# Kernel tuning notes

Measured on AMD Instinct MI355X. Metric: run time of the kernel, lower is better.

The kernel has to match this reference:

```python
import jax, jax.numpy as jnp
import numpy as np

B, V, J, NB = 512, 6890, 24, 10
P = (J - 1) * 9  # 207 pose-blendshape features

# Standard SMPL kinematic tree (root parent = -1)
SMPL_PARENTS = np.array([-1, 0, 0, 0, 1, 2, 3, 4, 5, 6, 7, 8, 9, 9, 9,
                         12, 13, 14, 16, 17, 18, 19, 20, 21], dtype=np.int32)


def setup_inputs() -> dict:
    key = jax.random.key(0)
    ks = jax.random.split(key, 7)
    betas = jax.random.normal(ks[0], (B, NB), jnp.float32)
    pose = 0.2 * jax.random.normal(ks[1], (B, J * 3), jnp.float32)
    v_template = jax.random.normal(ks[2], (V, 3), jnp.float32)
    shapedirs = 0.01 * jax.random.normal(ks[3], (V, 3, NB), jnp.float32)
    posedirs = 0.01 * jax.random.normal(ks[4], (P, V * 3), jnp.float32)
    J_regressor = jax.random.uniform(ks[5], (J, V), jnp.float32)
    J_regressor = J_regressor / jnp.sum(J_regressor, axis=1, keepdims=True)
    lbs_weights = jax.random.uniform(ks[6], (V, J), jnp.float32)
    lbs_weights = lbs_weights / jnp.sum(lbs_weights, axis=1, keepdims=True)
    parents = jnp.asarray(SMPL_PARENTS)
    return {"betas": betas, "pose": pose, "v_template": v_template,
            "shapedirs": shapedirs, "posedirs": posedirs,
            "J_regressor": J_regressor, "lbs_weights": lbs_weights,
            "parents": parents}


def batch_rodrigues(aa):
    """Axis-angle (N,3) -> rotation matrices (N,3,3), matching the torch impl."""
    angle = jnp.linalg.norm(aa + 1e-8, axis=1, keepdims=True)  # (N,1)
    rd = aa / angle
    cos = jnp.cos(angle)[:, :, None]  # (N,1,1)
    sin = jnp.sin(angle)[:, :, None]
    rx, ry, rz = rd[:, 0], rd[:, 1], rd[:, 2]
    zeros = jnp.zeros_like(rx)
    K = jnp.stack([zeros, -rz, ry,
                   rz, zeros, -rx,
                   -ry, rx, zeros], axis=1).reshape(-1, 3, 3)
    ident = jnp.eye(3, dtype=aa.dtype)
    return ident + sin * K + (1.0 - cos) * jnp.matmul(K, K)


def reference(betas, pose, v_template, shapedirs, posedirs, J_regressor,
              lbs_weights, parents):
    par = np.asarray(parents)  # static kinematic tree (host constants)
    b = betas.shape[0]
    nj = J_regressor.shape[0]
    # shape blendshapes: v_shaped = v_template + sum_l betas_l * shapedirs[...,l]
    v_shaped = v_template[None] + jnp.einsum('bl,vkl->bvk', betas, shapedirs)
    Jloc = jnp.einsum('bvk,jv->bjk', v_shaped, J_regressor)  # (b,J,3)
    rot = batch_rodrigues(pose.reshape(-1, 3)).reshape(b, nj, 3, 3)
    # pose blendshapes
    ident = jnp.eye(3, dtype=rot.dtype)
    pose_feature = (rot[:, 1:] - ident).reshape(b, -1)  # (b,207)
    v_posed = v_shaped + (pose_feature @ posedirs).reshape(b, -1, 3)
    # relative joint locations
    rel = Jloc.at[:, 1:].add(-Jloc[:, par[1:]])
    # per-joint local transforms (b,J,4,4)
    top = jnp.concatenate([rot, rel[..., None]], axis=-1)  # (b,J,3,4)
    bottom = jnp.broadcast_to(jnp.array([0., 0., 0., 1.], dtype=rot.dtype),
                              (b, nj, 1, 4))
    tm = jnp.concatenate([top, bottom], axis=2)
    # kinematic chain (fixed, tiny loop over 24 joints with static parents)
    chain = [tm[:, 0]]
    for i in range(1, par.shape[0]):
        chain.append(chain[par[i]] @ tm[:, i])
    transforms = jnp.stack(chain, axis=1)  # (b,J,4,4) absolute transforms
    posed_joints = transforms[:, :, :3, 3]
    # remove rest-pose joint offset: A = transforms - [0|transforms @ [J;0]]
    jh = jnp.concatenate([Jloc, jnp.zeros_like(Jloc[..., :1])], axis=-1)
    init_bone = jnp.einsum('bjpq,bjq->bjp', transforms, jh)  # (b,J,4)
    A = transforms - jnp.pad(init_bone[..., None], ((0, 0), (0, 0), (0, 0), (3, 0)))
    # linear blend skinning: per-vertex transform T = sum_j w_vj * A_j
    T = jnp.einsum('vj,bjpq->bvpq', lbs_weights, A)  # (b,V,4,4)
    verts = jnp.einsum('bvpk,bvk->bvp', T[:, :, :3, :3], v_posed) + T[:, :, :3, 3]
    return verts, posed_joints, A, transforms, v_posed
```

## Files before the change

### kernel.cpp

```cpp
#include <hip/hip_runtime.h>
#include <hip/hip_bf16.h>

#define BB 512
#define VV 6890
#define NJ 24
#define NBETA 10
#define NP 207
#define N3 (VV*3)
#define TBAT 32

#define OFF_VERTS 0
#define OFF_PJ   (BB*VV*3)
#define OFF_A    (OFF_PJ + BB*NJ*3)
#define OFF_TF   (OFF_A + BB*NJ*16)
#define OFF_VP   (OFF_TF + BB*NJ*16)

#define WS_JTJS 0
#define WS_PF   (WS_JTJS + NJ*33)
#define WS_A    (WS_PF + BB*NP)

__constant__ int c_par[NJ] = {-1, 0, 0, 0, 1, 2, 3, 4, 5, 6, 7, 8,
                              9, 9, 9, 12, 13, 14, 16, 17, 18, 19, 20, 21};

__global__ void k_jreg(const float* __restrict__ jr,
                       const float* __restrict__ vt,
                       const float* __restrict__ sd,
                       float* __restrict__ ws) {
    int j = blockIdx.x / 33, idx = blockIdx.x % 33;
    int t = threadIdx.x;
    float acc = 0.f;
    for (int v = t; v < VV; v += 256) {
        float a = jr[j * VV + v];
        float x = (idx < 3) ? vt[v * 3 + idx] : sd[v * 30 + (idx - 3)];
        acc += a * x;
    }
    __shared__ float red[256];
    red[t] = acc;
    __syncthreads();
    for (int s = 128; s > 0; s >>= 1) {
        if (t < s) red[t] += red[t + s];
        __syncthreads();
    }
    if (t == 0) ws[WS_JTJS + j * 33 + idx] = red[0];
}

__global__ __launch_bounds__(64) void k_chain(
        const float* __restrict__ betas,
        const float* __restrict__ pose,
        const float* __restrict__ ws_jtjs,
        float* __restrict__ ws_pf,
        float* __restrict__ ws_A,
        float* __restrict__ out) {
    int b = blockIdx.x;
    int t = threadIdx.x;
    __shared__ float Jl[NJ][3];
    __shared__ float tm[NJ][16];
    __shared__ float ch[NJ][16];
    float R[9];

    if (t < NJ) {
        int j = t;
        float bb[NBETA];
#pragma unroll
        for (int l = 0; l < NBETA; l++) bb[l] = betas[b * NBETA + l];
#pragma unroll
        for (int k = 0; k < 3; k++) {
            float acc = ws_jtjs[j * 33 + k];
#pragma unroll
            for (int l = 0; l < NBETA; l++) acc += bb[l] * ws_jtjs[j * 33 + 3 + k * NBETA + l];
            Jl[j][k] = acc;
        }
        float ax = pose[b * NJ * 3 + j * 3 + 0];
        float ay = pose[b * NJ * 3 + j * 3 + 1];
        float az = pose[b * NJ * 3 + j * 3 + 2];
        float e0 = ax + 1e-8f, e1 = ay + 1e-8f, e2 = az + 1e-8f;
        float ang = sqrtf(e0 * e0 + e1 * e1 + e2 * e2);
        float inv = 1.f / ang;
        float rx = ax * inv, ry = ay * inv, rz = az * inv;
        float sn = sinf(ang), cs = cosf(ang);
        float Km[9] = {0.f, -rz, ry, rz, 0.f, -rx, -ry, rx, 0.f};
#pragma unroll
        for (int r = 0; r < 3; r++)
#pragma unroll
            for (int c = 0; c < 3; c++) {
                float kk = Km[3 * r + 0] * Km[0 + c] + Km[3 * r + 1] * Km[3 + c] +
                           Km[3 * r + 2] * Km[6 + c];
                R[3 * r + c] = ((r == c) ? 1.f : 0.f) + sn * Km[3 * r + c] + (1.f - cs) * kk;
            }
        if (j >= 1) {
#pragma unroll
            for (int e = 0; e < 9; e++) {
                int r = e / 3, c = e % 3;
                ws_pf[b * NP + (j - 1) * 9 + e] = R[e] - ((r == c) ? 1.f : 0.f);
            }
        }
    }
    __syncthreads();
    if (t < NJ) {
        int j = t;
        int p = c_par[j];
        int ps = (p < 0) ? 0 : p;
#pragma unroll
        for (int r = 0; r < 3; r++) {
            tm[j][r * 4 + 0] = R[3 * r + 0];
            tm[j][r * 4 + 1] = R[3 * r + 1];
            tm[j][r * 4 + 2] = R[3 * r + 2];
            tm[j][r * 4 + 3] = (j == 0) ? Jl[j][r] : (Jl[j][r] - Jl[ps][r]);
        }
        tm[j][12] = 0.f; tm[j][13] = 0.f; tm[j][14] = 0.f; tm[j][15] = 1.f;
    }
    __syncthreads();
    if (t < 16) ch[0][t] = tm[0][t];
    __syncthreads();
    for (int i = 1; i < NJ; i++) {
        if (t < 16) {
            int r = t >> 2, c = t & 3;
            int p = c_par[i];
            ch[i][t] = ch[p][4 * r + 0] * tm[i][0 + c] + ch[p][4 * r + 1] * tm[i][4 + c] +
                       ch[p][4 * r + 2] * tm[i][8 + c] + ch[p][4 * r + 3] * tm[i][12 + c];
        }
        __syncthreads();
    }
    if (t < NJ) {
        int j = t;
        float ib[4];
#pragma unroll
        for (int p = 0; p < 4; p++)
            ib[p] = ch[j][4 * p + 0] * Jl[j][0] + ch[j][4 * p + 1] * Jl[j][1] +
                    ch[j][4 * p + 2] * Jl[j][2];
#pragma unroll
        for (int e = 0; e < 16; e++) {
            int r = e >> 2, c = e & 3;
            float tr = ch[j][e];
            float Ae = tr - ((c == 3) ? ib[r] : 0.f);
            out[OFF_TF + (size_t)(b * NJ + j) * 16 + e] = tr;
            out[OFF_A + (size_t)(b * NJ + j) * 16 + e] = Ae;
            ws_A[(size_t)(b * NJ + j) * 16 + e] = Ae;
        }
#pragma unroll
        for (int k = 0; k < 3; k++)
            out[OFF_PJ + (size_t)(b * NJ + j) * 3 + k] = ch[j][4 * k + 3];
    }
}

__global__ void k_posed(const float* __restrict__ vt,
                        const float* __restrict__ sd,
                        const float* __restrict__ betas,
                        const float* __restrict__ pd,
                        const float* __restrict__ ws_pf,
                        float* __restrict__ out) {
    int b0 = blockIdx.y * TBAT;
    int n0 = (blockIdx.x * 256 + threadIdx.x) * 2;
    __shared__ float pf[TBAT][NP];
    __shared__ float bbs[TBAT][NBETA];
    for (int idx = threadIdx.x; idx < TBAT * NP; idx += 256) {
        int bi = idx / NP, p = idx % NP;
        pf[bi][p] = ws_pf[(b0 + bi) * NP + p];
    }
    for (int idx = threadIdx.x; idx < TBAT * NBETA; idx += 256) {
        int bi = idx / NBETA, l = idx % NBETA;
        bbs[bi][l] = betas[(b0 + bi) * NBETA + l];
    }
    __syncthreads();
    if (n0 >= N3) return;
    float acc0[TBAT], acc1[TBAT];
#pragma unroll
    for (int bi = 0; bi < TBAT; bi++) { acc0[bi] = 0.f; acc1[bi] = 0.f; }
    for (int p0 = 0; p0 < NP; p0 += 9) {
        float pdv0[9], pdv1[9];
#pragma unroll
        for (int pc = 0; pc < 9; pc++) {
            const float2 v = *(const float2*)&pd[(size_t)(p0 + pc) * N3 + n0];
            pdv0[pc] = v.x; pdv1[pc] = v.y;
        }
#pragma unroll
        for (int bi = 0; bi < TBAT; bi++) {
#pragma unroll
            for (int pc = 0; pc < 9; pc++) {
                float w = pf[bi][p0 + pc];
                acc0[bi] += w * pdv0[pc];
                acc1[bi] += w * pdv1[pc];
            }
        }
    }
    float base0 = vt[n0], base1 = vt[n0 + 1];
    float sdv0[NBETA], sdv1[NBETA];
#pragma unroll
    for (int l = 0; l < NBETA; l++) { sdv0[l] = sd[n0 * NBETA + l]; sdv1[l] = sd[(n0 + 1) * NBETA + l]; }
#pragma unroll
    for (int bi = 0; bi < TBAT; bi++) {
        float s0 = base0 + acc0[bi], s1 = base1 + acc1[bi];
#pragma unroll
        for (int l = 0; l < NBETA; l++) { s0 += bbs[bi][l] * sdv0[l]; s1 += bbs[bi][l] * sdv1[l]; }
        float2 o; o.x = s0; o.y = s1;
        *(float2*)&out[OFF_VP + (size_t)(b0 + bi) * N3 + n0] = o;
    }
}

__global__ void k_verts(const float* __restrict__ lw,
                        const float* __restrict__ ws_A,
                        float* __restrict__ out) {
    int b = blockIdx.y;
    int v = blockIdx.x * 256 + threadIdx.x;
    __shared__ float A12[NJ][12];
    int t = threadIdx.x;
    for (int e = t; e < NJ * 12; e += 256) {
        int j = e / 12, rc = e % 12;
        A12[j][rc] = ws_A[(size_t)(b * NJ + j) * 16 + rc];
    }
    __syncthreads();
    if (v >= VV) return;
    float T[12];
#pragma unroll
    for (int e = 0; e < 12; e++) T[e] = 0.f;
#pragma unroll
    for (int j = 0; j < NJ; j++) {
        float wj = lw[v * NJ + j];
#pragma unroll
        for (int e = 0; e < 12; e++) T[e] += wj * A12[j][e];
    }
    size_t base = (size_t)(b * VV + v) * 3;
    float x = out[OFF_VP + base + 0];
    float y = out[OFF_VP + base + 1];
    float z = out[OFF_VP + base + 2];
#pragma unroll
    for (int p = 0; p < 3; p++) {
        out[OFF_VERTS + base + p] =
            T[4 * p + 0] * x + T[4 * p + 1] * y + T[4 * p + 2] * z + T[4 * p + 3];
    }
}

extern "C" void kernel_launch(void* const* d_in, const int* in_sizes, int n_in,
                              void* d_out, int out_size, void* d_ws, size_t ws_size,
                              hipStream_t stream) {
    const float* betas = (const float*)d_in[0];
    const float* pose  = (const float*)d_in[1];
    const float* vt    = (const float*)d_in[2];
    const float* sd    = (const float*)d_in[3];
    const float* pd    = (const float*)d_in[4];
    const float* jr    = (const float*)d_in[5];
    const float* lw    = (const float*)d_in[6];
    float* out = (float*)d_out;
    float* ws = (float*)d_ws;

    k_jreg<<<NJ * 33, 256, 0, stream>>>(jr, vt, sd, ws);
    k_chain<<<BB, 64, 0, stream>>>(betas, pose, ws + WS_JTJS, ws + WS_PF,
                                   ws + WS_A, out);
    k_posed<<<dim3((N3 / 2 + 255) / 256, BB / TBAT), 256, 0, stream>>>(
        vt, sd, betas, pd, ws + WS_PF, out);
    k_verts<<<dim3((VV + 255) / 256, BB), 256, 0, stream>>>(lw, ws + WS_A, out);
}
```

Measured before the change: 278.6 us.

## Read per-batch coefficients directly from global memory instead of LDS staging

Removes the shared-memory staging and barriers in k_posed and k_verts. Uniform per-batch data (pose features, betas, A matrices) is now read straight from global memory, where the compiler can use scalar loads since the addresses are block-uniform. k_posed's batch tile is halved and a launch bound is added to raise occupancy, and k_verts loads the skinning weights as float4. The trade-off is that posedirs must be re-read twice as often, because each block now covers fewer batches.

New measurement: 231.0 us. 17.1% less time.

```diff
diff --git a/kernel.cpp b/kernel.cpp
--- a/kernel.cpp
+++ b/kernel.cpp
@@ -7,7 +7,7 @@
 #define NBETA 10
 #define NP 207
 #define N3 (VV*3)
-#define TBAT 32
+#define TBAT 16
 
 #define OFF_VERTS 0
 #define OFF_PJ   (BB*VV*3)
@@ -143,29 +143,21 @@
     }
 }
 
-__global__ void k_posed(const float* __restrict__ vt,
-                        const float* __restrict__ sd,
-                        const float* __restrict__ betas,
-                        const float* __restrict__ pd,
-                        const float* __restrict__ ws_pf,
-                        float* __restrict__ out) {
+__global__ __launch_bounds__(256, 4) void k_posed(
+        const float* __restrict__ vt,
+        const float* __restrict__ sd,
+        const float* __restrict__ betas,
+        const float* __restrict__ pd,
+        const float* __restrict__ ws_pf,
+        float* __restrict__ out) {
     int b0 = blockIdx.y * TBAT;
     int n0 = (blockIdx.x * 256 + threadIdx.x) * 2;
-    __shared__ float pf[TBAT][NP];
-    __shared__ float bbs[TBAT][NBETA];
-    for (int idx = threadIdx.x; idx < TBAT * NP; idx += 256) {
-        int bi = idx / NP, p = idx % NP;
-        pf[bi][p] = ws_pf[(b0 + bi) * NP + p];
-    }
-    for (int idx = threadIdx.x; idx < TBAT * NBETA; idx += 256) {
-        int bi = idx / NBETA, l = idx % NBETA;
-        bbs[bi][l] = betas[(b0 + bi) * NBETA + l];
-    }
-    __syncthreads();
     if (n0 >= N3) return;
+
     float acc0[TBAT], acc1[TBAT];
 #pragma unroll
     for (int bi = 0; bi < TBAT; bi++) { acc0[bi] = 0.f; acc1[bi] = 0.f; }
+
     for (int p0 = 0; p0 < NP; p0 += 9) {
         float pdv0[9], pdv1[9];
 #pragma unroll
@@ -175,23 +167,33 @@
         }
 #pragma unroll
         for (int bi = 0; bi < TBAT; bi++) {
+            const float* __restrict__ pfr = &ws_pf[(size_t)(b0 + bi) * NP + p0];
 #pragma unroll
             for (int pc = 0; pc < 9; pc++) {
-                float w = pf[bi][p0 + pc];
+                float w = pfr[pc];
                 acc0[bi] += w * pdv0[pc];
                 acc1[bi] += w * pdv1[pc];
             }
         }
     }
+
     float base0 = vt[n0], base1 = vt[n0 + 1];
     float sdv0[NBETA], sdv1[NBETA];
 #pragma unroll
-    for (int l = 0; l < NBETA; l++) { sdv0[l] = sd[n0 * NBETA + l]; sdv1[l] = sd[(n0 + 1) * NBETA + l]; }
+    for (int l = 0; l < NBETA; l++) {
+        sdv0[l] = sd[(size_t)n0 * NBETA + l];
+        sdv1[l] = sd[(size_t)(n0 + 1) * NBETA + l];
+    }
 #pragma unroll
     for (int bi = 0; bi < TBAT; bi++) {
+        const float* __restrict__ br = &betas[(size_t)(b0 + bi) * NBETA];
         float s0 = base0 + acc0[bi], s1 = base1 + acc1[bi];
 #pragma unroll
-        for (int l = 0; l < NBETA; l++) { s0 += bbs[bi][l] * sdv0[l]; s1 += bbs[bi][l] * sdv1[l]; }
+        for (int l = 0; l < NBETA; l++) {
+            float bl = br[l];
+            s0 += bl * sdv0[l];
+            s1 += bl * sdv1[l];
+        }
         float2 o; o.x = s0; o.y = s1;
         *(float2*)&out[OFF_VP + (size_t)(b0 + bi) * N3 + n0] = o;
     }
@@ -202,23 +204,27 @@
                         float* __restrict__ out) {
     int b = blockIdx.y;
     int v = blockIdx.x * 256 + threadIdx.x;
-    __shared__ float A12[NJ][12];
-    int t = threadIdx.x;
-    for (int e = t; e < NJ * 12; e += 256) {
-        int j = e / 12, rc = e % 12;
-        A12[j][rc] = ws_A[(size_t)(b * NJ + j) * 16 + rc];
-    }
-    __syncthreads();
     if (v >= VV) return;
+
+    float wv[NJ];
+#pragma unroll
+    for (int j0 = 0; j0 < NJ; j0 += 4) {
+        const float4 w4 = *(const float4*)&lw[(size_t)v * NJ + j0];
+        wv[j0 + 0] = w4.x; wv[j0 + 1] = w4.y; wv[j0 + 2] = w4.z; wv[j0 + 3] = w4.w;
+    }
+
     float T[12];
 #pragma unroll
     for (int e = 0; e < 12; e++) T[e] = 0.f;
+    const float* __restrict__ Ab = ws_A + (size_t)b * NJ * 16;
 #pragma unroll
     for (int j = 0; j < NJ; j++) {
-        float wj = lw[v * NJ + j];
-#pragma unroll
-        for (int e = 0; e < 12; e++) T[e] += wj * A12[j][e];
-    }
+        const float* __restrict__ Aj = Ab + j * 16;
+        float wj = wv[j];
+#pragma unroll
+        for (int e = 0; e < 12; e++) T[e] += wj * Aj[e];
+    }
+
     size_t base = (size_t)(b * VV + v) * 3;
     float x = out[OFF_VP + base + 0];
     float y = out[OFF_VP + base + 1];
```
